# Optimization experiments

Measured on AMD Instinct MI355X. Metric: run time of the kernel, lower is better.

The kernel has to match this reference:

```python
import jax, jax.numpy as jnp
import numpy as np

N_NODES = 10000
N_EDGES = 640000
D_IN = 128
D_OUT = 128


def setup_inputs() -> dict:
    key = jax.random.key(0)
    k_x, k_src, k_dst, k_w, k_b = jax.random.split(key, 5)
    x = jax.random.normal(k_x, (N_NODES, D_IN), dtype=jnp.float32)
    src = jax.random.randint(k_src, (N_EDGES,), 0, N_NODES, dtype=jnp.int64)
    dst = jax.random.randint(k_dst, (N_EDGES,), 0, N_NODES, dtype=jnp.int64)
    # nn.Linear default init: U(-1/sqrt(fan_in), 1/sqrt(fan_in))
    bound = 1.0 / np.sqrt(D_IN)
    W = jax.random.uniform(k_w, (D_OUT, D_IN), minval=-bound, maxval=bound, dtype=jnp.float32)
    b = jax.random.uniform(k_b, (D_OUT,), minval=-bound, maxval=bound, dtype=jnp.float32)
    return {"x": x, "src": src, "dst": dst, "W": W, "b": b}


def reference(x, src, dst, W, b):
    # Message passing: gather source-node features per edge, scatter-sum to dst.
    msg = x[src]  # [E, D_IN]
    h = jax.ops.segment_sum(msg, dst, num_segments=N_NODES)  # [N, D_IN]
    # Dense linear: h @ W.T + b
    return jnp.einsum("nd,od->no", h, W) + b
```

## Files before the change

### kernel.cpp

```cpp
#include <hip/hip_runtime.h>
#include <hip/hip_bf16.h>
#include <stdint.h>


#define NBLK 256
#define CBSH 4
#define CBSZ 16
#define NCMAX 640
#define CAP 28
#define MAXE 1408

typedef __attribute__((ext_vector_type(8))) short bf16x8;
typedef __attribute__((ext_vector_type(4))) float f32x4;

static __device__ inline unsigned short f2bf(float f) {
    unsigned int u = __float_as_uint(f);
    u += 0x7fffu + ((u >> 16) & 1u);
    return (unsigned short)(u >> 16);
}

__global__ __launch_bounds__(512) void k_fused(const float* __restrict__ x,
                                               const float* __restrict__ W,
                                               unsigned short* __restrict__ y,
                                               int N, int xwb,
                                               const void* __restrict__ srcv,
                                               const void* __restrict__ dstv,
                                               unsigned int* __restrict__ staging,
                                               unsigned short* __restrict__ cnts,
                                               int NC, int E, int C) {
    __shared__ uint4 shbuf[2048];
    __shared__ unsigned int shAny;
    int t = threadIdx.x;
    if ((int)blockIdx.x < NBLK) {
        int* cur = (int*)shbuf;
        if (t == 0) shAny = 0u;
        __syncthreads();
        if (t < 256) {
            unsigned int v = ((const unsigned int*)srcv)[2 * t + 1];
            if (v) atomicOr(&shAny, 1u);
        }
        int bid = blockIdx.x;
        for (int i = t; i < NC; i += 512) cur[i] = (bid * NC + i) * CAP;
        __syncthreads();
        int f64 = shAny ? 0 : 1;
        int beg = bid * C, end = min(E, beg + C);
        int nfull = (end - beg) & ~3;
        if (f64) {
            const long long* s = (const long long*)srcv;
            const long long* d = (const long long*)dstv;
            for (int e0 = beg + 4 * t; e0 < beg + nfull; e0 += 4 * 512) {
                ulonglong2 dA = *(const ulonglong2*)(d + e0);
                ulonglong2 dB = *(const ulonglong2*)(d + e0 + 2);
                ulonglong2 sA = *(const ulonglong2*)(s + e0);
                ulonglong2 sB = *(const ulonglong2*)(s + e0 + 2);
                int dv[4] = {(int)dA.x, (int)dA.y, (int)dB.x, (int)dB.y};
                int sv[4] = {(int)sA.x, (int)sA.y, (int)sB.x, (int)sB.y};
#pragma unroll
                for (int j = 0; j < 4; ++j) {
                    int cb = dv[j] >> CBSH;
                    int pos = atomicAdd(&cur[cb], 1);
                    if (pos - (bid * NC + cb) * CAP < CAP)
                        staging[pos] = ((unsigned int)(dv[j] & (CBSZ - 1)) << 16) |
                                       (unsigned int)sv[j];
                }
            }
            int te = beg + nfull + t;
            if (te < end) {
                int dv = (int)d[te];
                int cb = dv >> CBSH;
                int pos = atomicAdd(&cur[cb], 1);
                if (pos - (bid * NC + cb) * CAP < CAP)
                    staging[pos] = ((unsigned int)(dv & (CBSZ - 1)) << 16) |
                                   (unsigned int)(int)s[te];
            }
        } else {
            const int* s = (const int*)srcv;
            const int* d = (const int*)dstv;
            for (int e0 = beg + 4 * t; e0 < beg + nfull; e0 += 4 * 512) {
                uint4 d4 = *(const uint4*)(d + e0);
                uint4 s4 = *(const uint4*)(s + e0);
                int dv[4] = {(int)d4.x, (int)d4.y, (int)d4.z, (int)d4.w};
                int sv[4] = {(int)s4.x, (int)s4.y, (int)s4.z, (int)s4.w};
#pragma unroll
                for (int j = 0; j < 4; ++j) {
                    int cb = dv[j] >> CBSH;
                    int pos = atomicAdd(&cur[cb], 1);
                    if (pos - (bid * NC + cb) * CAP < CAP)
                        staging[pos] = ((unsigned int)(dv[j] & (CBSZ - 1)) << 16) |
                                       (unsigned int)sv[j];
                }
            }
            int te = beg + nfull + t;
            if (te < end) {
                int dv = d[te];
                int cb = dv >> CBSH;
                int pos = atomicAdd(&cur[cb], 1);
                if (pos - (bid * NC + cb) * CAP < CAP)
                    staging[pos] = ((unsigned int)(dv & (CBSZ - 1)) << 16) |
                                   (unsigned int)s[te];
            }
        }
        __syncthreads();
        for (int i = t; i < NC; i += 512) {
            int cnt = cur[i] - (bid * NC + i) * CAP;
            if (cnt > CAP) cnt = CAP;
            cnts[(size_t)i * NBLK + bid] = (unsigned short)cnt;
        }
    } else {
        for (int i = t; i < 2048; i += 512) {
            int o = i >> 4, g = i & 15;
            const float4* wp = (const float4*)(W + o * 128 + g * 8);
            float4 f0 = wp[0], f1 = wp[1];
            uint4 pk;
            pk.x = (unsigned int)f2bf(f0.x) | ((unsigned int)f2bf(f0.y) << 16);
            pk.y = (unsigned int)f2bf(f0.z) | ((unsigned int)f2bf(f0.w) << 16);
            pk.z = (unsigned int)f2bf(f1.x) | ((unsigned int)f2bf(f1.y) << 16);
            pk.w = (unsigned int)f2bf(f1.z) | ((unsigned int)f2bf(f1.w) << 16);
            shbuf[o * 16 + (g ^ (o & 15))] = pk;
        }
        __syncthreads();
        int wid = (blockIdx.x - NBLK) * 8 + (t >> 6);
        int lane = t & 63;
        int m0 = wid * 16;
        if (m0 >= N) return;
        int r = lane & 15, hi = lane >> 4;
        int mr = m0 + r; if (mr >= N) mr = N - 1;
        bf16x8 a[4];
        const float* xr = x + (size_t)mr * 128 + hi * 8;
#pragma unroll
        for (int kt = 0; kt < 4; ++kt) {
            float4 f0 = *(const float4*)(xr + kt * 32);
            float4 f1 = *(const float4*)(xr + kt * 32 + 4);
            unsigned short* ap = (unsigned short*)&a[kt];
            ap[0]=f2bf(f0.x); ap[1]=f2bf(f0.y); ap[2]=f2bf(f0.z); ap[3]=f2bf(f0.w);
            ap[4]=f2bf(f1.x); ap[5]=f2bf(f1.y); ap[6]=f2bf(f1.z); ap[7]=f2bf(f1.w);
        }
#pragma unroll 2
        for (int ot = 0; ot < 8; ++ot) {
            f32x4 acc = {0.f, 0.f, 0.f, 0.f};
            int o = ot * 16 + r;
#pragma unroll
            for (int kt = 0; kt < 4; ++kt) {
                uint4 wv4 = shbuf[o * 16 + ((kt * 4 + hi) ^ (o & 15))];
                bf16x8 bf;
                *(uint4*)&bf = wv4;
                acc = __builtin_amdgcn_mfma_f32_16x16x32_bf16(a[kt], bf, acc, 0, 0, 0);
            }
#pragma unroll
            for (int reg = 0; reg < 4; ++reg) {
                int m = m0 + hi * 4 + reg;
                if (m < N) y[(size_t)m * 128 + ot * 16 + r] = f2bf(acc[reg]);
            }
        }
    }
}

__global__ __launch_bounds__(512) void k_sortgather(const unsigned int* __restrict__ staging,
                                                    const unsigned short* __restrict__ cnts,
                                                    const unsigned short* __restrict__ y,
                                                    const float* __restrict__ bias,
                                                    float* __restrict__ out,
                                                    int N, int NC) {
    __shared__ unsigned int eLds[MAXE];
    __shared__ unsigned short sorted[MAXE];
    __shared__ int wcnt[NBLK], woff[NBLK];
    __shared__ int lbE[CBSZ], cuA[CBSZ];
    __shared__ int Msh;
    int c = blockIdx.x, t = threadIdx.x;
    int wv = t >> 6, lane = t & 63;
    if (t < 64) {
        uint2 pv = ((const uint2*)(cnts + (size_t)c * NBLK))[t];
        int c0 = (int)(pv.x & 0xFFFFu), c1 = (int)(pv.x >> 16);
        int c2 = (int)(pv.y & 0xFFFFu), c3 = (int)(pv.y >> 16);
        int s = c0 + c1 + c2 + c3;
        int incl = s;
#pragma unroll
        for (int off = 1; off < 64; off <<= 1) {
            int u = __shfl_up(incl, off);
            if (t >= off) incl += u;
        }
        int excl = incl - s;
        wcnt[4*t] = c0; wcnt[4*t+1] = c1; wcnt[4*t+2] = c2; wcnt[4*t+3] = c3;
        woff[4*t] = excl; woff[4*t+1] = excl + c0;
        woff[4*t+2] = excl + c0 + c1; woff[4*t+3] = excl + c0 + c1 + c2;
        if (t == 63) Msh = incl;
    }
    if (t >= 64 && t < 64 + CBSZ) lbE[t - 64] = 0;
    __syncthreads();
    int M = Msh; if (M > MAXE) M = MAXE;
    int gq = t >> 2, ln4 = t & 3;
#pragma unroll
    for (int i = 0; i < 2; ++i) {
        int k = gq + i * 128;
        int cw = wcnt[k];
        int base = woff[k];
        const unsigned int* srcw = staging + ((size_t)k * NC + c) * CAP;
        for (int j = ln4; j < cw; j += 4) {
            int dp = base + j;
            if (dp < MAXE) eLds[dp] = srcw[j];
        }
    }
    __syncthreads();
    for (int i = t; i < M; i += 512) atomicAdd(&lbE[eLds[i] >> 16], 1);
    __syncthreads();
    if (t < CBSZ) {
        int v = lbE[t];
        int incl = v;
#pragma unroll
        for (int off = 1; off < CBSZ; off <<= 1) {
            int u = __shfl_up(incl, off);
            if (t >= off) incl += u;
        }
        lbE[t] = incl - v;
        cuA[t] = incl - v;
    }
    __syncthreads();
    for (int i = t; i < M; i += 512) {
        unsigned int p = eLds[i];
        int pos = atomicAdd(&cuA[p >> 16], 1);
        if (pos < MAXE) sorted[pos] = (unsigned short)(p & 0xFFFFu);
    }
    __syncthreads();
    int r = lane & 15, g = lane >> 4;
    const uint4* yp = (const uint4*)y;
#pragma unroll
    for (int q = 0; q < 2; ++q) {
        int tloc = wv * 2 + q;
        int node = (c << CBSH) + tloc;
        if (node >= N) continue;
        int beg = lbE[tloc];
        int lcnt = cuA[tloc] - beg;
        float2 a0 = {0.f,0.f}, a1 = {0.f,0.f}, a2 = {0.f,0.f}, a3 = {0.f,0.f};
        int nb4 = lcnt >> 2;
#pragma unroll 4
        for (int k = 0; k < nb4; ++k) {
            int sid = (int)sorted[beg + 4 * k + g];
            uint4 v = yp[(size_t)sid * 16 + r];
            a0.x += __uint_as_float(v.x << 16); a0.y += __uint_as_float(v.x & 0xffff0000u);
            a1.x += __uint_as_float(v.y << 16); a1.y += __uint_as_float(v.y & 0xffff0000u);
            a2.x += __uint_as_float(v.z << 16); a2.y += __uint_as_float(v.z & 0xffff0000u);
            a3.x += __uint_as_float(v.w << 16); a3.y += __uint_as_float(v.w & 0xffff0000u);
        }
        int idx = (nb4 << 2) + g;
        if (idx < lcnt) {
            int sid = (int)sorted[beg + idx];
            uint4 v = yp[(size_t)sid * 16 + r];
            a0.x += __uint_as_float(v.x << 16); a0.y += __uint_as_float(v.x & 0xffff0000u);
            a1.x += __uint_as_float(v.y << 16); a1.y += __uint_as_float(v.y & 0xffff0000u);
            a2.x += __uint_as_float(v.z << 16); a2.y += __uint_as_float(v.z & 0xffff0000u);
            a3.x += __uint_as_float(v.w << 16); a3.y += __uint_as_float(v.w & 0xffff0000u);
        }
        a0.x += __shfl_xor(a0.x, 16); a0.x += __shfl_xor(a0.x, 32);
        a0.y += __shfl_xor(a0.y, 16); a0.y += __shfl_xor(a0.y, 32);
        a1.x += __shfl_xor(a1.x, 16); a1.x += __shfl_xor(a1.x, 32);
        a1.y += __shfl_xor(a1.y, 16); a1.y += __shfl_xor(a1.y, 32);
        a2.x += __shfl_xor(a2.x, 16); a2.x += __shfl_xor(a2.x, 32);
        a2.y += __shfl_xor(a2.y, 16); a2.y += __shfl_xor(a2.y, 32);
        a3.x += __shfl_xor(a3.x, 16); a3.x += __shfl_xor(a3.x, 32);
        a3.y += __shfl_xor(a3.y, 16); a3.y += __shfl_xor(a3.y, 32);
        if (lane < 16) {
            float4 b0 = ((const float4*)bias)[r * 2];
            float4 b1 = ((const float4*)bias)[r * 2 + 1];
            float4 o0 = {a0.x + b0.x, a0.y + b0.y, a1.x + b0.z, a1.y + b0.w};
            float4 o1 = {a2.x + b1.x, a2.y + b1.y, a3.x + b1.z, a3.y + b1.w};
            float4* op = (float4*)(out + (size_t)node * 128 + r * 8);
            op[0] = o0;
            op[1] = o1;
        }
    }
}

extern "C" void kernel_launch(void* const* d_in, const int* in_sizes, int n_in,
                              void* d_out, int out_size, void* d_ws, size_t ws_size,
                              hipStream_t stream) {
    const float* x = (const float*)d_in[0];
    const void* srcv = d_in[1];
    const void* dstv = d_in[2];
    const float* W = (const float*)d_in[3];
    const float* bias = (const float*)d_in[4];
    float* out = (float*)d_out;

    const int D = 128;
    int N = in_sizes[0] / D;
    int E = in_sizes[1];
    int C = (E + NBLK - 1) / NBLK;
    int NC = (N + CBSZ - 1) >> CBSH;

    char* ws = (char*)d_ws;
    size_t off = 0;
    auto take = [&](size_t bytes) {
        char* p = ws + off;
        off = (off + bytes + 255) & ~(size_t)255;
        return p;
    };
    unsigned short* y      = (unsigned short*)take((size_t)N * D * 2);
    unsigned int* staging  = (unsigned int*)take((size_t)NBLK * NC * CAP * 4);
    unsigned short* cnts   = (unsigned short*)take((size_t)NC * NBLK * 2);

    int xwb = (((N + 15) / 16) + 7) / 8;

    k_fused<<<NBLK + xwb, 512, 0, stream>>>(x, W, y, N, xwb, srcv, dstv,
                                            staging, cnts, NC, E, C);
    k_sortgather<<<NC, 512, 0, stream>>>(staging, cnts, y, bias, out, N, NC);
}
```

Baseline: 34.43 us.

## Replace LDS counting sort with direct per-node bucket slots and halve producer blocks

The sort-gather kernel no longer stages edges into LDS, counts them, scans, and scatters. Each edge is now appended straight into a fixed-capacity per-node bucket in shared memory through an atomic counter. This removes two passes and several barriers. The producer block count drops from 256 to 128 and the per-bucket staging capacity grows to match, which changes the fused kernel's partitioning and adds a risk of overflow truncation if a node exceeds 192 incoming edges.

```diff
diff --git a/kernel.cpp b/kernel.cpp
--- a/kernel.cpp
+++ b/kernel.cpp
@@ -3,12 +3,12 @@
 #include <stdint.h>
 
 
-#define NBLK 256
+#define NBLK 128
 #define CBSH 4
 #define CBSZ 16
 #define NCMAX 640
-#define CAP 28
-#define MAXE 1408
+#define CAP 44
+#define CAPN 192
 
 typedef __attribute__((ext_vector_type(8))) short bf16x8;
 typedef __attribute__((ext_vector_type(4))) float f32x4;
@@ -161,66 +161,33 @@
                                                     const float* __restrict__ bias,
                                                     float* __restrict__ out,
                                                     int N, int NC) {
-    __shared__ unsigned int eLds[MAXE];
-    __shared__ unsigned short sorted[MAXE];
-    __shared__ int wcnt[NBLK], woff[NBLK];
-    __shared__ int lbE[CBSZ], cuA[CBSZ];
-    __shared__ int Msh;
+    __shared__ unsigned short sorted[CBSZ * CAPN];
+    __shared__ int wcnt[NBLK];
+    __shared__ int nodeCnt[CBSZ];
     int c = blockIdx.x, t = threadIdx.x;
+    if (t < 64) {
+        unsigned int pv = ((const unsigned int*)(cnts + (size_t)c * NBLK))[t];
+        wcnt[2 * t] = (int)(pv & 0xFFFFu);
+        wcnt[2 * t + 1] = (int)(pv >> 16);
+    }
+    if (t >= 64 && t < 64 + CBSZ) nodeCnt[t - 64] = 0;
+    __syncthreads();
+    int gq = t >> 3, ln8 = t & 7;
+#pragma unroll
+    for (int i = 0; i < 2; ++i) {
+        int k = gq + i * 64;
+        int cw = wcnt[k];
+        const unsigned int* srcw = staging + ((size_t)k * NC + c) * CAP;
+        for (int j = ln8; j < cw; j += 8) {
+            unsigned int p = srcw[j];
+            int node = (int)(p >> 16);
+            int pos = atomicAdd(&nodeCnt[node], 1);
+            if (pos < CAPN)
+                sorted[node * CAPN + pos] = (unsigned short)(p & 0xFFFFu);
+        }
+    }
+    __syncthreads();
     int wv = t >> 6, lane = t & 63;
-    if (t < 64) {
-        uint2 pv = ((const uint2*)(cnts + (size_t)c * NBLK))[t];
-        int c0 = (int)(pv.x & 0xFFFFu), c1 = (int)(pv.x >> 16);
-        int c2 = (int)(pv.y & 0xFFFFu), c3 = (int)(pv.y >> 16);
-        int s = c0 + c1 + c2 + c3;
-        int incl = s;
-#pragma unroll
-        for (int off = 1; off < 64; off <<= 1) {
-            int u = __shfl_up(incl, off);
-            if (t >= off) incl += u;
-        }
-        int excl = incl - s;
-        wcnt[4*t] = c0; wcnt[4*t+1] = c1; wcnt[4*t+2] = c2; wcnt[4*t+3] = c3;
-        woff[4*t] = excl; woff[4*t+1] = excl + c0;
-        woff[4*t+2] = excl + c0 + c1; woff[4*t+3] = excl + c0 + c1 + c2;
-        if (t == 63) Msh = incl;
-    }
-    if (t >= 64 && t < 64 + CBSZ) lbE[t - 64] = 0;
-    __syncthreads();
-    int M = Msh; if (M > MAXE) M = MAXE;
-    int gq = t >> 2, ln4 = t & 3;
-#pragma unroll
-    for (int i = 0; i < 2; ++i) {
-        int k = gq + i * 128;
-        int cw = wcnt[k];
-        int base = woff[k];
-        const unsigned int* srcw = staging + ((size_t)k * NC + c) * CAP;
-        for (int j = ln4; j < cw; j += 4) {
-            int dp = base + j;
-            if (dp < MAXE) eLds[dp] = srcw[j];
-        }
-    }
-    __syncthreads();
-    for (int i = t; i < M; i += 512) atomicAdd(&lbE[eLds[i] >> 16], 1);
-    __syncthreads();
-    if (t < CBSZ) {
-        int v = lbE[t];
-        int incl = v;
-#pragma unroll
-        for (int off = 1; off < CBSZ; off <<= 1) {
-            int u = __shfl_up(incl, off);
-            if (t >= off) incl += u;
-        }
-        lbE[t] = incl - v;
-        cuA[t] = incl - v;
-    }
-    __syncthreads();
-    for (int i = t; i < M; i += 512) {
-        unsigned int p = eLds[i];
-        int pos = atomicAdd(&cuA[p >> 16], 1);
-        if (pos < MAXE) sorted[pos] = (unsigned short)(p & 0xFFFFu);
-    }
-    __syncthreads();
     int r = lane & 15, g = lane >> 4;
     const uint4* yp = (const uint4*)y;
 #pragma unroll
@@ -228,13 +195,13 @@
         int tloc = wv * 2 + q;
         int node = (c << CBSH) + tloc;
         if (node >= N) continue;
-        int beg = lbE[tloc];
-        int lcnt = cuA[tloc] - beg;
+        int lcnt = nodeCnt[tloc]; if (lcnt > CAPN) lcnt = CAPN;
+        const unsigned short* sl = sorted + tloc * CAPN;
         float2 a0 = {0.f,0.f}, a1 = {0.f,0.f}, a2 = {0.f,0.f}, a3 = {0.f,0.f};
         int nb4 = lcnt >> 2;
 #pragma unroll 4
         for (int k = 0; k < nb4; ++k) {
-            int sid = (int)sorted[beg + 4 * k + g];
+            int sid = (int)sl[4 * k + g];
             uint4 v = yp[(size_t)sid * 16 + r];
             a0.x += __uint_as_float(v.x << 16); a0.y += __uint_as_float(v.x & 0xffff0000u);
             a1.x += __uint_as_float(v.y << 16); a1.y += __uint_as_float(v.y & 0xffff0000u);
@@ -243,7 +210,7 @@
         }
         int idx = (nb4 << 2) + g;
         if (idx < lcnt) {
-            int sid = (int)sorted[beg + idx];
+            int sid = (int)sl[idx];
             uint4 v = yp[(size_t)sid * 16 + r];
             a0.x += __uint_as_float(v.x << 16); a0.y += __uint_as_float(v.x & 0xffff0000u);
             a1.x += __uint_as_float(v.y << 16); a1.y += __uint_as_float(v.y & 0xffff0000u);
```

Result: faster. 29.80 us, median of 3 (-13.4%).
